# Performance work log

Measured on AMD Instinct MI355X. Metric: run time of the kernel, lower is better.

The kernel has to match this reference:

```python
import jax, jax.numpy as jnp
import numpy as np

E = 512   # embed_size == hidden_size (required: step-0 'embed' is the init output of size hidden)
H = 512
A = 512   # attention dim
V = 20000
P = 196
B = 128
T = 24


def setup_inputs() -> dict:
    key = jax.random.key(0)
    ks = jax.random.split(key, 20)
    s = 0.02
    return {
        "features": jax.random.normal(ks[0], (B, P, E), jnp.float32),
        "captions": jax.random.randint(ks[1], (B, T), 0, V),
        "emb": jax.random.normal(ks[2], (V, E), jnp.float32) * s,
        "W_init_h": jax.random.normal(ks[3], (E, H), jnp.float32) * s,
        "b_init_h": jnp.zeros((H,), jnp.float32),
        "W_init_o": jax.random.normal(ks[4], (E, H), jnp.float32) * s,
        "b_init_o": jnp.zeros((H,), jnp.float32),
        "Wf": jax.random.normal(ks[5], (E, A), jnp.float32) * s,
        "bf": jnp.zeros((A,), jnp.float32),
        "Wh": jax.random.normal(ks[6], (H, A), jnp.float32) * s,
        "bh": jnp.zeros((A,), jnp.float32),
        "v_att": jax.random.normal(ks[7], (A,), jnp.float32) * s,
        "W_ih": jax.random.normal(ks[8], (3 * H, 2 * E), jnp.float32) * s,
        "W_hh": jax.random.normal(ks[9], (3 * H, H), jnp.float32) * s,
        "b_ih": jnp.zeros((3 * H,), jnp.float32),
        "b_hh": jnp.zeros((3 * H,), jnp.float32),
        "W_out": jax.random.normal(ks[10], (V, H), jnp.float32) * s,
        "b_out": jnp.zeros((V,), jnp.float32),
    }


def reference(features, emb, W_init_h, b_init_h, W_init_o, b_init_o,
              Wf, bf, Wh, bh, v_att, W_ih, W_hh, b_ih, b_hh,
              W_out, b_out, captions):
    # init_hidden_state
    avg = features.mean(axis=1)                          # [B,E]
    hidden0 = jnp.tanh(avg @ W_init_h + b_init_h)        # [B,H]
    output0 = jnp.tanh(avg @ W_init_o + b_init_o)        # [B,H]

    emb_caps = emb[captions]                             # [B,T,E]
    # teacher forcing: step 0 uses init output, step i>0 uses embeddings[:, i-1]
    embed_seq = jnp.concatenate([output0[:, None, :], emb_caps[:, :-1, :]], axis=1)
    xs = embed_seq.transpose(1, 0, 2)                    # [T,B,E]

    feat_proj = features @ Wf + bf                       # [B,P,A] (precompute attn key proj)

    def step(h, x_emb):
        # additive attention over pixels
        score = jnp.tanh(feat_proj + (h @ Wh + bh)[:, None, :]) @ v_att   # [B,P]
        alpha = jax.nn.softmax(score, axis=1)
        ctx = jnp.einsum('bp,bpe->be', alpha, features)                   # [B,E]
        x = jnp.concatenate([x_emb, ctx], axis=1)                         # [B,2E]
        # single-step GRU (PyTorch gate order r,z,n)
        gi = x @ W_ih.T + b_ih
        gh = h @ W_hh.T + b_hh
        gi_r, gi_z, gi_n = jnp.split(gi, 3, axis=1)
        gh_r, gh_z, gh_n = jnp.split(gh, 3, axis=1)
        r = jax.nn.sigmoid(gi_r + gh_r)
        z = jax.nn.sigmoid(gi_z + gh_z)
        n = jnp.tanh(gi_n + r * gh_n)
        h_new = (1.0 - z) * n + z * h
        pred = h_new @ W_out.T + b_out                                    # [B,V]
        return h_new, pred

    _, preds = jax.lax.scan(step, hidden0, xs)           # preds: [T,B,V]
    return preds.transpose(1, 0, 2)                      # [B,T,V]
```

## Files before the change

kernel.cpp:

```cpp
#include <hip/hip_runtime.h>

#define Bb 128
#define Tt 24
#define Ee 512
#define Hh 512
#define Aa 512
#define Vv 20000
#define Pp 196
#define TV (Tt*Vv)
#define NBLK 512
#define NTHR 256
#define GT (NBLK*NTHR)

typedef __attribute__((ext_vector_type(8))) short bfrag;
typedef __attribute__((ext_vector_type(4))) float f4;
typedef __attribute__((ext_vector_type(4))) unsigned short us4;

#define MFMA16(a,b,c) __builtin_amdgcn_mfma_f32_16x16x32_bf16(a,b,c,0,0,0)

__device__ __forceinline__ unsigned short f2bf(float f){
  unsigned int x = __builtin_bit_cast(unsigned int, f);
  x += 0x7fffu + ((x >> 16) & 1u);
  return (unsigned short)(x >> 16);
}
__device__ __forceinline__ float bfu2f(unsigned short u){
  unsigned int x = ((unsigned int)u) << 16;
  return __builtin_bit_cast(float, x);
}
#define LOG2E 1.442695041f
__device__ __forceinline__ float fexp2(float x){ return __builtin_amdgcn_exp2f(x); }
__device__ __forceinline__ float frcp (float x){ return __builtin_amdgcn_rcpf(x); }
__device__ __forceinline__ float tanh_f(float x){ return 1.0f - 2.0f*frcp(1.0f + fexp2((2.0f*LOG2E)*x)); }
__device__ __forceinline__ float sigm_f(float x){ return frcp(1.0f + fexp2(-LOG2E*x)); }

__device__ __forceinline__ unsigned long long scld8(const void* p){
  return __hip_atomic_load((const unsigned long long*)p, __ATOMIC_RELAXED, __HIP_MEMORY_SCOPE_AGENT);
}
__device__ __forceinline__ unsigned scld4(const unsigned* p){
  return __hip_atomic_load(p, __ATOMIC_RELAXED, __HIP_MEMORY_SCOPE_AGENT);
}
__device__ __forceinline__ void scst4(unsigned* p, unsigned v){
  __hip_atomic_store(p, v, __ATOMIC_RELAXED, __HIP_MEMORY_SCOPE_AGENT);
}

__device__ __forceinline__ void set_flag(unsigned* line, unsigned v){
  asm volatile("s_waitcnt vmcnt(0)" ::: "memory");
  __syncthreads();
  if(threadIdx.x == 0) scst4(line, v);
}
__device__ __forceinline__ void poll_flags(const unsigned* base, int n, unsigned tgt){
  int tid = threadIdx.x;
  for(;;){
    int ok = (tid < n) ? (scld4(base + tid*16) >= tgt) : 1;
    if(__syncthreads_count(ok) == NTHR) break;
    __builtin_amdgcn_s_sleep(4);
  }
  asm volatile("" ::: "memory");
}

__device__ __forceinline__ void gbar2(unsigned* sync, unsigned phase){
  __syncthreads();
  int tid = threadIdx.x, blk = blockIdx.x;
  if(tid == 0)
    (void)__hip_atomic_fetch_add(sync + (blk & 31)*16, 1u,
                                 __ATOMIC_RELEASE, __HIP_MEMORY_SCOPE_AGENT);
  if(blk == 0){
    for(;;){
      int ok = (tid < 32) ? (scld4(sync + tid*16) >= phase*16u) : 1;
      if(__syncthreads_count(ok) == NTHR) break;
      __builtin_amdgcn_s_sleep(2);
    }
    if(tid == 0) scst4(sync + 32*16, phase);
  }
  if(tid == 0){
    while(scld4(sync + 32*16) < phase) __builtin_amdgcn_s_sleep(2);
    (void)__hip_atomic_load(sync + 32*16, __ATOMIC_ACQUIRE, __HIP_MEMORY_SCOPE_AGENT);
  }
  __syncthreads();
}

__global__ void k_zero(unsigned* s){
  int i = blockIdx.x*256 + threadIdx.x;
  s[i] = 0u;
}

__device__ __forceinline__ void cast_loop(const float* __restrict__ s,
                                          unsigned short* __restrict__ d,
                                          int n4, int gtid){
  for(int i = gtid; i < n4; i += GT){
    float4 v = ((const float4*)s)[i];
    us4 o; o[0]=f2bf(v.x); o[1]=f2bf(v.y); o[2]=f2bf(v.z); o[3]=f2bf(v.w);
    ((us4*)d)[i] = o;
  }
}
__device__ __forceinline__ void tr_tile(const float* __restrict__ S,
                                        unsigned short* __restrict__ D,
                                        int it, int jt, int tid, float (*T)[33]){
  int er = tid>>3, c4 = (tid&7)*4;
  float4 v = *(const float4*)(S + (size_t)(jt*32+er)*512 + it*32 + c4);
  T[er][c4+0]=v.x; T[er][c4+1]=v.y; T[er][c4+2]=v.z; T[er][c4+3]=v.w;
  __syncthreads();
  us4 o;
  o[0]=f2bf(T[c4+0][er]); o[1]=f2bf(T[c4+1][er]);
  o[2]=f2bf(T[c4+2][er]); o[3]=f2bf(T[c4+3][er]);
  *(us4*)(D + (size_t)(it*32+er)*512 + jt*32 + c4) = o;
  __syncthreads();
}

__device__ __forceinline__ void stage16(char* dstSM, const unsigned short* src, int R0){
  int tid = threadIdx.x;
  #pragma unroll
  for(int j=0;j<8;j++){
    int u = tid + j*256;
    int row = u >> 7, c8 = u & 127;
    unsigned long long q = scld8(src + (size_t)(R0+row)*Hh + c8*4);
    int bo = (row<<10) + (c8<<3);
    bo ^= (row&7)<<4;
    *(unsigned long long*)(dstSM + bo) = q;
  }
}


__device__ void attention_task(int b, const unsigned short* __restrict__ hbU_t,
                               const unsigned short* __restrict__ WhT, const float* __restrict__ bhv,
                               const unsigned short* __restrict__ fpb,
                               const unsigned short* __restrict__ featsB,
                               const float* __restrict__ vatt,
                               unsigned short* __restrict__ ctx_t, char* SM)
{
  float* h_s = (float*)SM;
  float* hp  = h_s + 512;
  float* vp  = hp + 512;
  float* sc  = vp + 512;
  float* red = sc + 200;
  int tid = threadIdx.x;
  if(tid < 128){
    unsigned long long q8 = scld8(hbU_t + (size_t)b*Hh + tid*4);
    h_s[tid*4+0] = bfu2f((unsigned short)(q8));
    h_s[tid*4+1] = bfu2f((unsigned short)(q8>>16));
    h_s[tid*4+2] = bfu2f((unsigned short)(q8>>32));
    h_s[tid*4+3] = bfu2f((unsigned short)(q8>>48));
  }
  { float2 vv = *(const float2*)(vatt + tid*2);
    int a0=tid*2, a1=a0+1;
    vp[((a0&31)<<4)+(a0>>5)] = vv.x;
    vp[((a1&31)<<4)+(a1>>5)] = vv.y; }
  __syncthreads();
  for(int rep=0;rep<2;rep++){
    int a = tid + rep*256;
    float s = bhv[a];
    const unsigned short* wr = WhT + (size_t)a*Hh;
    for(int k=0;k<Hh;k+=8){
      bfrag wv = *(const bfrag*)(wr + k);
      #pragma unroll
      for(int q=0;q<8;q++) s += h_s[k+q] * bfu2f((unsigned short)wv[q]);
    }
    hp[((a&31)<<4)+(a>>5)] = s;
  }
  __syncthreads();
  int grp = tid >> 4, gl = tid & 15;
  for(int pass=0; pass<13; pass++){
    int p = pass*16 + grp;
    float acc = 0.0f;
    if(p < Pp){
      const unsigned short* fr = fpb + ((size_t)b*Pp + p)*Aa + gl*32;
      #pragma unroll
      for(int j=0;j<32;j+=8){
        bfrag fv = *(const bfrag*)(fr + j);
        #pragma unroll
        for(int q=0;q<8;q++){
          int idx = ((j+q)<<4) + gl;
          float x = bfu2f((unsigned short)fv[q]) + hp[idx];
          acc += tanh_f(x) * vp[idx];
        }
      }
    }
    acc += __shfl_xor(acc, 1, 64);
    acc += __shfl_xor(acc, 2, 64);
    acc += __shfl_xor(acc, 4, 64);
    acc += __shfl_xor(acc, 8, 64);
    if(p < Pp && gl == 0) sc[p] = acc;
  }
  __syncthreads();
  if(tid < 64){
    float m = -1e30f;
    for(int i=0;i<4;i++){ int p = tid + i*64; if(p < Pp) m = fmaxf(m, sc[p]); }
    for(int off=1; off<64; off<<=1) m = fmaxf(m, __shfl_xor(m, off, 64));
    float s = 0.0f;
    for(int i=0;i<4;i++){ int p = tid + i*64; if(p < Pp) s += fexp2((sc[p]-m)*LOG2E); }
    for(int off=1; off<64; off<<=1) s += __shfl_xor(s, off, 64);
    if(tid == 0){ red[0] = m; red[1] = frcp(s); }
  }
  __syncthreads();
  float mx = red[0], rS = red[1];
  float al_t = 0.0f;
  if(tid < Pp) al_t = fexp2((sc[tid]-mx)*LOG2E) * rS;
  __syncthreads();
  if(tid < Pp) sc[tid] = al_t;
  __syncthreads();
  float c0 = 0.f, c1 = 0.f;
  const unsigned int* fb = (const unsigned int*)(featsB + (size_t)b*Pp*Ee);
  for(int p=0;p<Pp;p++){
    float al = sc[p];
    unsigned int u = fb[(size_t)p*256 + tid];
    unsigned int lo = (u & 0xffffu) << 16, hi = u & 0xffff0000u;
    c0 += al * __builtin_bit_cast(float, lo);
    c1 += al * __builtin_bit_cast(float, hi);
  }
  unsigned int cw = ((unsigned int)f2bf(c1) << 16) | (unsigned int)f2bf(c0);
  scst4((unsigned*)ctx_t + (size_t)b*256 + tid, cw);
}

__device__ void gates_phaseA(int R0, int HC0, const unsigned short* __restrict__ eseqT,
                             const unsigned short* __restrict__ WihB,
                             const unsigned short* __restrict__ WhhB,
                             const char* SMh, f4 (&agh)[3], f4 (&agi)[3])
{
  int tid = threadIdx.x;
  int w = tid>>6, l = tid&63, l16 = l&15, lk = l>>4;
  int hcol = HC0 + w*16 + l16;
  #pragma unroll
  for(int q=0;q<3;q++){ agh[q]=(f4)(0.f); agi[q]=(f4)(0.f); }
  for(int k0=0;k0<512;k0+=32){
    int koff = k0 + lk*8;
    int bo = (l16<<10) + (koff<<1); bo ^= (l16&7)<<4;
    bfrag ah = *(const bfrag*)(SMh + bo);
    bfrag ae = *(const bfrag*)(eseqT + (size_t)(R0+l16)*Ee + koff);
    #pragma unroll
    for(int q=0;q<3;q++){
      int j = q*512 + hcol;
      bfrag bh_ = *(const bfrag*)(WhhB + (size_t)j*512  + koff);
      bfrag be  = *(const bfrag*)(WihB + (size_t)j*1024 + koff);
      agh[q] = MFMA16(ah, bh_, agh[q]);
      agi[q] = MFMA16(ae, be,  agi[q]);
    }
  }
}

__device__ void gates_phaseB(int R0, int HC0, const char* SMc,
                             const unsigned short* __restrict__ WihB,
                             const float* __restrict__ bih, const float* __restrict__ bhh,
                             const float* __restrict__ hf_cur, float* __restrict__ hf_nxt,
                             unsigned short* __restrict__ hbU_nxt,
                             f4 (&agh)[3], f4 (&agi)[3], char* SM_HB)
{
  int tid = threadIdx.x;
  int w = tid>>6, l = tid&63, l16 = l&15, lk = l>>4;
  int hcol = HC0 + w*16 + l16;
  for(int k0=0;k0<512;k0+=32){
    int koff = k0 + lk*8;
    int bo = (l16<<10) + (koff<<1); bo ^= (l16&7)<<4;
    bfrag ac = *(const bfrag*)(SMc + bo);
    #pragma unroll
    for(int q=0;q<3;q++){
      int j = q*512 + hcol;
      bfrag bc = *(const bfrag*)(WihB + (size_t)j*1024 + 512 + koff);
      agi[q] = MFMA16(ac, bc, agi[q]);
    }
  }
  float bir = bih[hcol],      bhr = bhh[hcol];
  float biz = bih[512+hcol],  bhz = bhh[512+hcol];
  float bin = bih[1024+hcol], bhn = bhh[1024+hcol];
  unsigned short (*HB)[64] = (unsigned short(*)[64])SM_HB;
  #pragma unroll
  for(int i=0;i<4;i++){
    int row = lk*4 + i;
    int b = R0 + row;
    float r_ = sigm_f(agi[0][i] + bir + agh[0][i] + bhr);
    float z_ = sigm_f(agi[1][i] + biz + agh[1][i] + bhz);
    float n_ = tanh_f(agi[2][i] + bin + r_*(agh[2][i] + bhn));
    float ho = hf_cur[(size_t)b*Hh + hcol];
    float hn = (1.0f - z_)*n_ + z_*ho;
    hf_nxt[(size_t)b*Hh + hcol] = hn;
    HB[row][w*16 + l16] = f2bf(hn);
  }
  __syncthreads();
  #pragma unroll
  for(int j=0;j<2;j++){
    int widx = tid + j*256;
    int row = widx >> 5, pr = widx & 31;
    unsigned uu = (unsigned)HB[row][pr*2] | ((unsigned)HB[row][pr*2+1] << 16);
    scst4((unsigned*)(hbU_nxt + (size_t)(R0+row)*Hh + HC0) + pr, uu);
  }
}

__device__ void pred_task(int pt, int tw, const unsigned short* __restrict__ hb_cur,
                          const unsigned short* __restrict__ WoutB,
                          const float* __restrict__ bout, float* __restrict__ out,
                          char* SM)
{
  int tid = threadIdx.x;
  int vchunk = pt >> 1, mbase = (pt & 1)*64;
  for(int j=0;j<32;j++){
    int u = tid + j*256;
    int row = u >> 7, c8 = u & 127;
    unsigned long long q = scld8(hb_cur + (size_t)(mbase+row)*Hh + c8*4);
    int bo = (row<<10) + (c8<<3);
    bo ^= (row&7)<<4;
    *(unsigned long long*)(SM + bo) = q;
  }
  __syncthreads();
  int w = tid>>6, l = tid&63, l16 = l&15, lk = l>>4;
  int nb = vchunk*128 + w*32;
  f4 acc[4][2];
  #pragma unroll
  for(int mi=0;mi<4;mi++) for(int ni=0;ni<2;ni++) acc[mi][ni] = (f4)(0.0f);
  for(int k0=0;k0<512;k0+=32){
    int koff = k0 + lk*8;
    bfrag af[4], bq[2];
    #pragma unroll
    for(int mi=0;mi<4;mi++){
      int row = mi*16 + l16;
      int bo = (row<<10) + (koff<<1);
      bo ^= (row&7)<<4;
      af[mi] = *(const bfrag*)(SM + bo);
    }
    #pragma unroll
    for(int ni=0;ni<2;ni++){
      int v = nb + ni*16 + l16; if(v > Vv-1) v = Vv-1;
      bq[ni] = *(const bfrag*)(WoutB + (size_t)v*Hh + koff);
    }
    #pragma unroll
    for(int mi=0;mi<4;mi++)
      #pragma unroll
      for(int ni=0;ni<2;ni++)
        acc[mi][ni] = MFMA16(af[mi], bq[ni], acc[mi][ni]);
  }
  #pragma unroll
  for(int ni=0;ni<2;ni++){
    int v = nb + ni*16 + l16;
    if(v < Vv){
      float bias = bout[v];
      #pragma unroll
      for(int mi=0;mi<4;mi++){
        #pragma unroll
        for(int i=0;i<4;i++){
          int br = mbase + mi*16 + lk*4 + i;
          __builtin_nontemporal_store(acc[mi][ni][i] + bias,
              out + (size_t)br*TV + (size_t)tw*Vv + v);
        }
      }
    }
  }
  __syncthreads();
}

__global__ __launch_bounds__(NTHR, 2) void k_all(
    const float* feats, const int* caps, const float* emb,
    const float* Winh, const float* binh, const float* Wino, const float* bino,
    const float* Wf, const float* bfv, const float* Wh, const float* bhv,
    const float* vatt, const float* Wih, const float* Whh,
    const float* bih, const float* bhh, const float* Wout, const float* bout,
    float* out,
    float* hfR, unsigned short* hbU,
    unsigned short* ctxR, unsigned short* avgB, unsigned short* eseq,
    unsigned short* WfT, unsigned short* WhT,
    unsigned short* WinhT, unsigned short* WinoT,
    unsigned short* WihB, unsigned short* WhhB,
    unsigned short* fpb, unsigned short* featsB, unsigned short* WoutB,
    unsigned* sync)
{
  __shared__ char SMEM[65536];
  const int blk = blockIdx.x, tid = threadIdx.x;
  const int gtid = blk*NTHR + tid;
  unsigned* flagsA = sync + 40*16;
  unsigned* flagsG = sync + 168*16;
  unsigned* aggP   = sync + 240*16;
  float* h_f0 = hfR;
  unsigned short* h_b0 = hbU;

  cast_loop(Wih,  WihB,  (3*Hh*2*Ee)/4, gtid);
  cast_loop(Whh,  WhhB,  (3*Hh*Hh)/4,   gtid);
  cast_loop(Wout, WoutB, (Vv*Hh)/4,     gtid);
  cast_loop(feats,featsB,(Bb*Pp*Ee)/4,  gtid);
  for(int task = blk; task < 1024; task += NBLK){
    int z = task >> 8, rt = task & 255;
    int it = rt & 15, jt = rt >> 4;
    const float* S = (z==0)?Wf:(z==1)?Wh:(z==2)?Winh:Wino;
    unsigned short* D = (z==0)?WfT:(z==1)?WhT:(z==2)?WinhT:WinoT;
    tr_tile(S, D, it, jt, tid, (float(*)[33])SMEM);
  }
  if(blk < Bb){
    int b = blk;
    const float* fb = feats + (size_t)b*Pp*Ee;
    float a0=0.f, a1=0.f;
    for(int p=0;p<Pp;p++){
      float2 v = *(const float2*)(fb + (size_t)p*Ee + tid*2);
      a0 += v.x; a1 += v.y;
    }
    a0 *= (1.0f/Pp); a1 *= (1.0f/Pp);
    unsigned int pack = ((unsigned int)f2bf(a1)<<16) | (unsigned int)f2bf(a0);
    ((unsigned int*)avgB)[(size_t)b*256 + tid] = pack;
  }
  for(int task = blk; task < (Tt-1)*Bb; task += NBLK){
    int ts = task/Bb + 1, b = task%Bb;
    int cap = caps[b*Tt + (ts-1)];
    float2 v = *(const float2*)(emb + (size_t)cap*Ee + tid*2);
    unsigned int pack = ((unsigned int)f2bf(v.y)<<16) | (unsigned int)f2bf(v.x);
    ((unsigned int*)(eseq + ((size_t)ts*Bb + b)*Ee))[tid] = pack;
  }
  gbar2(sync, 1);

  for(int task = blk; task < 1584; task += NBLK){
    int w = tid>>6, l = tid&63, l16 = l&15, lk = l>>4;
    if(task < 1568){
      int bx = task % 196, by = task / 196;
      size_t m_base = (size_t)bx*128 + (w&1)*64;
      int nb = by*64 + (w>>1)*32;
      f4 acc[4][2];
      #pragma unroll
      for(int mi=0;mi<4;mi++) for(int ni=0;ni<2;ni++) acc[mi][ni] = (f4)(0.0f);
      for(int k0=0;k0<512;k0+=32){
        int koff = k0 + lk*8;
        bfrag af[4], bq[2];
        #pragma unroll
        for(int mi=0;mi<4;mi++) af[mi] = *(const bfrag*)(featsB + (m_base+mi*16+l16)*512 + koff);
        #pragma unroll
        for(int ni=0;ni<2;ni++) bq[ni] = *(const bfrag*)(WfT + (size_t)(nb+ni*16+l16)*512 + koff);
        #pragma unroll
        for(int mi=0;mi<4;mi++)
          #pragma unroll
          for(int ni=0;ni<2;ni++)
            acc[mi][ni] = MFMA16(af[mi], bq[ni], acc[mi][ni]);
      }
      #pragma unroll
      for(int ni=0;ni<2;ni++){
        int a = nb + ni*16 + l16;
        float bias = bfv[a];
        #pragma unroll
        for(int mi=0;mi<4;mi++){
          size_t r = m_base + mi*16 + lk*4;
          #pragma unroll
          for(int i=0;i<4;i++)
            fpb[(r+i)*512 + a] = f2bf(acc[mi][ni][i] + bias);
        }
      }
    } else {
      int idx = task - 1568;
      int y = idx >> 3, xb = idx & 7;
      int m0 = (w&1)*64, nb = xb*64 + (w>>1)*32;
      const unsigned short* Wt = y ? WinoT : WinhT;
      const float* bias = y ? bino : binh;
      f4 acc[4][2];
      #pragma unroll
      for(int mi=0;mi<4;mi++) for(int ni=0;ni<2;ni++) acc[mi][ni] = (f4)(0.0f);
      for(int k0=0;k0<512;k0+=32){
        int koff = k0 + lk*8;
        bfrag af[4], bq[2];
        #pragma unroll
        for(int mi=0;mi<4;mi++) af[mi] = *(const bfrag*)(avgB + (size_t)(m0+mi*16+l16)*512 + koff);
        #pragma unroll
        for(int ni=0;ni<2;ni++) bq[ni] = *(const bfrag*)(Wt + (size_t)(nb+ni*16+l16)*512 + koff);
        #pragma unroll
        for(int mi=0;mi<4;mi++)
          #pragma unroll
          for(int ni=0;ni<2;ni++)
            acc[mi][ni] = MFMA16(af[mi], bq[ni], acc[mi][ni]);
      }
      #pragma unroll
      for(int ni=0;ni<2;ni++){
        int n = nb + ni*16 + l16;
        float bv = bias[n];
        #pragma unroll
        for(int mi=0;mi<4;mi++){
          int bb = m0 + mi*16 + lk*4;
          #pragma unroll
          for(int i=0;i<4;i++){
            float val = tanh_f(acc[mi][ni][i] + bv);
            if(y==0){ h_f0[(size_t)(bb+i)*Hh + n] = val; h_b0[(size_t)(bb+i)*Hh + n] = f2bf(val); }
            else    { eseq[(size_t)(bb+i)*Ee + n] = f2bf(val); }
          }
        }
      }
    }
  }
  gbar2(sync, 2);

  int xcd = blk & 7, slot = blk >> 3;

  if(slot < 16){
    int b = slot*8 + xcd;
    int rg = b >> 4;
    for(int t=0; t<Tt; t++){
      if(t > 0) poll_flags(flagsG + rg*8*16, 8, (unsigned)t);
      attention_task(b, hbU + (size_t)t*Bb*Hh, WhT, bhv, fpb, featsB, vatt,
                     ctxR + (size_t)(t&3)*Bb*Ee, SMEM);
      set_flag(flagsA + b*16, (unsigned)(t+1));
    }
  } else if(slot < 24){
    int r = slot - 16, c = xcd;
    int R0 = r*16, HC0 = c*64;
    char* SMh = SMEM;
    char* SMc = SMEM + 16384;
    char* SMB = SMEM + 32768;
    f4 agh[3], agi[3];
    stage16(SMh, hbU, R0);
    __syncthreads();
    gates_phaseA(R0, HC0, eseq, WihB, WhhB, SMh, agh, agi);
    for(int t=0; t<Tt; t++){
      poll_flags(flagsA + R0*16, 16, (unsigned)(t+1));
      stage16(SMc, ctxR + (size_t)(t&3)*Bb*Ee, R0);
      __syncthreads();
      gates_phaseB(R0, HC0, SMc, WihB, bih, bhh,
                   hfR + (size_t)(t&1)*Bb*Hh, hfR + (size_t)((t+1)&1)*Bb*Hh,
                   hbU + (size_t)(t+1)*Bb*Hh, agh, agi, SMB);
      set_flag(flagsG + (r*8+c)*16, (unsigned)(t+1));
      if(t+1 < Tt){
        poll_flags(flagsG + r*8*16, 8, (unsigned)(t+1));
        stage16(SMh, hbU + (size_t)(t+1)*Bb*Hh, R0);
        __syncthreads();
        gates_phaseA(R0, HC0, eseq + (size_t)(t+1)*Bb*Ee, WihB, WhhB, SMh, agh, agi);
      }
    }
  } else {
    int ps = slot - 24;
    int pt = xcd*40 + ps;
    if(ps == 0){
      for(int t=1; t<=Tt; t++){
        poll_flags(flagsG, 64, (unsigned)t);
        if(tid == 0) scst4(aggP + xcd*16, (unsigned)t);
        pred_task(pt, t-1, hbU + (size_t)t*Bb*Hh, WoutB, bout, out, SMEM);
      }
    } else if(pt < 314){
      for(int t=1; t<=Tt; t++){
        poll_flags(aggP + xcd*16, 1, (unsigned)t);
        pred_task(pt, t-1, hbU + (size_t)t*Bb*Hh, WoutB, bout, out, SMEM);
      }
    }
  }
}

extern "C" void kernel_launch(void* const* d_in, const int* in_sizes, int n_in,
                              void* d_out, int out_size, void* d_ws, size_t ws_size,
                              hipStream_t stream)
{
  const float* feats = (const float*)d_in[0];
  const int*   caps  = (const int*)d_in[1];
  const float* emb   = (const float*)d_in[2];
  const float* Winh  = (const float*)d_in[3];
  const float* binh  = (const float*)d_in[4];
  const float* Wino  = (const float*)d_in[5];
  const float* bino  = (const float*)d_in[6];
  const float* Wf    = (const float*)d_in[7];
  const float* bfv   = (const float*)d_in[8];
  const float* Wh    = (const float*)d_in[9];
  const float* bhv   = (const float*)d_in[10];
  const float* vatt  = (const float*)d_in[11];
  const float* Wih   = (const float*)d_in[12];
  const float* Whh   = (const float*)d_in[13];
  const float* bih   = (const float*)d_in[14];
  const float* bhh   = (const float*)d_in[15];
  const float* Wout  = (const float*)d_in[16];
  const float* bout  = (const float*)d_in[17];
  float* out = (float*)d_out;

  char* ws = (char*)d_ws;
  size_t off = 0;
  auto alloc = [&](size_t bytes){
    off = (off + 255) & ~(size_t)255;
    void* p = ws + off; off += bytes; return p;
  };
  unsigned* syncp = (unsigned*)alloc(16384);
  float* hfR = (float*)alloc((size_t)2*Bb*Hh*4);
  unsigned short* hbU = (unsigned short*)alloc((size_t)(Tt+1)*Bb*Hh*2);
  unsigned short* ctxR  = (unsigned short*)alloc((size_t)4*Bb*Ee*2);
  unsigned short* avgB  = (unsigned short*)alloc((size_t)Bb*Ee*2);
  unsigned short* eseq  = (unsigned short*)alloc((size_t)Tt*Bb*Ee*2);
  unsigned short* WfT   = (unsigned short*)alloc((size_t)Ee*Aa*2);
  unsigned short* WhT   = (unsigned short*)alloc((size_t)Hh*Aa*2);
  unsigned short* WinhT = (unsigned short*)alloc((size_t)Ee*Hh*2);
  unsigned short* WinoT = (unsigned short*)alloc((size_t)Ee*Hh*2);
  unsigned short* WihB  = (unsigned short*)alloc((size_t)3*Hh*2*Ee*2);
  unsigned short* WhhB  = (unsigned short*)alloc((size_t)3*Hh*Hh*2);
  unsigned short* fpb   = (unsigned short*)alloc((size_t)Bb*Pp*Aa*2);
  unsigned short* featsB= (unsigned short*)alloc((size_t)Bb*Pp*Ee*2);
  unsigned short* WoutB = (unsigned short*)alloc((size_t)Vv*Hh*2);
  if(ws_size < off) return;

  k_zero<<<16, 256, 0, stream>>>(syncp);
  k_all<<<NBLK, NTHR, 0, stream>>>(
      feats, caps, emb, Winh, binh, Wino, bino, Wf, bfv, Wh, bhv, vatt,
      Wih, Whh, bih, bhh, Wout, bout, out,
      hfR, hbU, ctxR, avgB, eseq,
      WfT, WhT, WinhT, WinoT, WihB, WhhB, fpb, featsB, WoutB, syncp);
}
```

Baseline: 1.676 ms.

## Move attention h-projection into GRU blocks via MFMA and reshape pred tiles

The per-batch scalar h@Wh projection inside each attention task is removed. The GRU tile blocks now compute it with MFMA right after staging h, write it to a double-buffered fp32 buffer, and publish a new flag that attention blocks poll. The prediction task switches from 64-row by 128-vocab tiles to 32-row by 256-vocab tiles, and launch bounds are raised to 4 blocks per CU with dynamic shared memory sized 34816 bytes. This cuts redundant projection work from the serial attention critical path, at the cost of an extra flag handshake and possible register pressure at the higher occupancy target.

```diff
diff --git a/kernel.cpp b/kernel.cpp
--- a/kernel.cpp
+++ b/kernel.cpp
@@ -11,6 +11,7 @@
 #define NBLK 512
 #define NTHR 256
 #define GT (NBLK*NTHR)
+#define SMEM_BYTES 34816
 
 typedef __attribute__((ext_vector_type(8))) short bfrag;
 typedef __attribute__((ext_vector_type(4))) float f4;
@@ -40,6 +41,9 @@
   return __hip_atomic_load(p, __ATOMIC_RELAXED, __HIP_MEMORY_SCOPE_AGENT);
 }
 __device__ __forceinline__ void scst4(unsigned* p, unsigned v){
+  __hip_atomic_store(p, v, __ATOMIC_RELAXED, __HIP_MEMORY_SCOPE_AGENT);
+}
+__device__ __forceinline__ void scstf(float* p, float v){
   __hip_atomic_store(p, v, __ATOMIC_RELAXED, __HIP_MEMORY_SCOPE_AGENT);
 }
 
@@ -121,41 +125,26 @@
 }
 
 
-__device__ void attention_task(int b, const unsigned short* __restrict__ hbU_t,
-                               const unsigned short* __restrict__ WhT, const float* __restrict__ bhv,
+__device__ void attention_task(int b, const float* __restrict__ hpr_t,
                                const unsigned short* __restrict__ fpb,
                                const unsigned short* __restrict__ featsB,
                                const float* __restrict__ vatt,
                                unsigned short* __restrict__ ctx_t, char* SM)
 {
-  float* h_s = (float*)SM;
-  float* hp  = h_s + 512;
+  float* hp  = (float*)SM;
   float* vp  = hp + 512;
   float* sc  = vp + 512;
   float* red = sc + 200;
   int tid = threadIdx.x;
-  if(tid < 128){
-    unsigned long long q8 = scld8(hbU_t + (size_t)b*Hh + tid*4);
-    h_s[tid*4+0] = bfu2f((unsigned short)(q8));
-    h_s[tid*4+1] = bfu2f((unsigned short)(q8>>16));
-    h_s[tid*4+2] = bfu2f((unsigned short)(q8>>32));
-    h_s[tid*4+3] = bfu2f((unsigned short)(q8>>48));
-  }
-  { float2 vv = *(const float2*)(vatt + tid*2);
-    int a0=tid*2, a1=a0+1;
+  {
+    unsigned long long q = scld8(hpr_t + (size_t)b*Aa + tid*2);
+    float2 hv = __builtin_bit_cast(float2, q);
+    float2 vv = *(const float2*)(vatt + tid*2);
+    int a0 = tid*2, a1 = a0+1;
+    hp[((a0&31)<<4)+(a0>>5)] = hv.x;
+    hp[((a1&31)<<4)+(a1>>5)] = hv.y;
     vp[((a0&31)<<4)+(a0>>5)] = vv.x;
-    vp[((a1&31)<<4)+(a1>>5)] = vv.y; }
-  __syncthreads();
-  for(int rep=0;rep<2;rep++){
-    int a = tid + rep*256;
-    float s = bhv[a];
-    const unsigned short* wr = WhT + (size_t)a*Hh;
-    for(int k=0;k<Hh;k+=8){
-      bfrag wv = *(const bfrag*)(wr + k);
-      #pragma unroll
-      for(int q=0;q<8;q++) s += h_s[k+q] * bfu2f((unsigned short)wv[q]);
-    }
-    hp[((a&31)<<4)+(a>>5)] = s;
+    vp[((a1&31)<<4)+(a1>>5)] = vv.y;
   }
   __syncthreads();
   int grp = tid >> 4, gl = tid & 15;
@@ -209,6 +198,29 @@
   }
   unsigned int cw = ((unsigned int)f2bf(c1) << 16) | (unsigned int)f2bf(c0);
   scst4((unsigned*)ctx_t + (size_t)b*256 + tid, cw);
+}
+
+__device__ void hproj_mfma(int R0, int HC0, const char* SMh,
+                           const unsigned short* __restrict__ WhT,
+                           const float* __restrict__ bhv, float* __restrict__ hpr)
+{
+  int tid = threadIdx.x;
+  int w = tid>>6, l = tid&63, l16 = l&15, lk = l>>4;
+  int a = HC0 + w*16 + l16;
+  f4 acc = (f4)(0.0f);
+  for(int k0=0;k0<512;k0+=32){
+    int koff = k0 + lk*8;
+    int bo = (l16<<10) + (koff<<1); bo ^= (l16&7)<<4;
+    bfrag ah = *(const bfrag*)(SMh + bo);
+    bfrag bq = *(const bfrag*)(WhT + (size_t)a*Hh + koff);
+    acc = MFMA16(ah, bq, acc);
+  }
+  float bias = bhv[a];
+  #pragma unroll
+  for(int i=0;i<4;i++){
+    int row = lk*4 + i;
+    scstf(hpr + (size_t)(R0+row)*Aa + a, acc[i] + bias);
+  }
 }
 
 __device__ void gates_phaseA(int R0, int HC0, const unsigned short* __restrict__ eseqT,
@@ -284,14 +296,15 @@
   }
 }
 
-__device__ void pred_task(int pt, int tw, const unsigned short* __restrict__ hb_cur,
-                          const unsigned short* __restrict__ WoutB,
-                          const float* __restrict__ bout, float* __restrict__ out,
-                          char* SM)
+__device__ void pred_task32(int pt, int tw, const unsigned short* __restrict__ hb_cur,
+                            const unsigned short* __restrict__ WoutB,
+                            const float* __restrict__ bout, float* __restrict__ out,
+                            char* SM)
 {
   int tid = threadIdx.x;
-  int vchunk = pt >> 1, mbase = (pt & 1)*64;
-  for(int j=0;j<32;j++){
+  int vchunk = pt >> 2, mbase = (pt & 3)*32;
+  #pragma unroll
+  for(int j=0;j<16;j++){
     int u = tid + j*256;
     int row = u >> 7, c8 = u & 127;
     unsigned long long q = scld8(hb_cur + (size_t)(mbase+row)*Hh + c8*4);
@@ -301,38 +314,38 @@
   }
   __syncthreads();
   int w = tid>>6, l = tid&63, l16 = l&15, lk = l>>4;
-  int nb = vchunk*128 + w*32;
-  f4 acc[4][2];
-  #pragma unroll
-  for(int mi=0;mi<4;mi++) for(int ni=0;ni<2;ni++) acc[mi][ni] = (f4)(0.0f);
+  int nb = vchunk*256 + w*64;
+  f4 acc[2][4];
+  #pragma unroll
+  for(int mi=0;mi<2;mi++) for(int ni=0;ni<4;ni++) acc[mi][ni] = (f4)(0.0f);
   for(int k0=0;k0<512;k0+=32){
     int koff = k0 + lk*8;
-    bfrag af[4], bq[2];
+    bfrag af[2], bq[4];
     #pragma unroll
-    for(int mi=0;mi<4;mi++){
+    for(int mi=0;mi<2;mi++){
       int row = mi*16 + l16;
       int bo = (row<<10) + (koff<<1);
       bo ^= (row&7)<<4;
       af[mi] = *(const bfrag*)(SM + bo);
     }
     #pragma unroll
-    for(int ni=0;ni<2;ni++){
+    for(int ni=0;ni<4;ni++){
       int v = nb + ni*16 + l16; if(v > Vv-1) v = Vv-1;
       bq[ni] = *(const bfrag*)(WoutB + (size_t)v*Hh + koff);
     }
     #pragma unroll
-    for(int mi=0;mi<4;mi++)
+    for(int mi=0;mi<2;mi++)
       #pragma unroll
-      for(int ni=0;ni<2;ni++)
+      for(int ni=0;ni<4;ni++)
         acc[mi][ni] = MFMA16(af[mi], bq[ni], acc[mi][ni]);
   }
   #pragma unroll
-  for(int ni=0;ni<2;ni++){
+  for(int ni=0;ni<4;ni++){
     int v = nb + ni*16 + l16;
     if(v < Vv){
       float bias = bout[v];
       #pragma unroll
-      for(int mi=0;mi<4;mi++){
+      for(int mi=0;mi<2;mi++){
         #pragma unroll
         for(int i=0;i<4;i++){
           int br = mbase + mi*16 + lk*4 + i;
@@ -345,14 +358,14 @@
   __syncthreads();
 }
 
-__global__ __launch_bounds__(NTHR, 2) void k_all(
+__global__ __launch_bounds__(NTHR, 4) void k_all(
     const float* feats, const int* caps, const float* emb,
     const float* Winh, const float* binh, const float* Wino, const float* bino,
     const float* Wf, const float* bfv, const float* Wh, const float* bhv,
     const float* vatt, const float* Wih, const float* Whh,
     const float* bih, const float* bhh, const float* Wout, const float* bout,
     float* out,
-    float* hfR, unsigned short* hbU,
+    float* hfR, unsigned short* hbU, float* hpr,
     unsigned short* ctxR, unsigned short* avgB, unsigned short* eseq,
     unsigned short* WfT, unsigned short* WhT,
     unsigned short* WinhT, unsigned short* WinoT,
@@ -360,12 +373,13 @@
     unsigned short* fpb, unsigned short* featsB, unsigned short* WoutB,
     unsigned* sync)
 {
-  __shared__ char SMEM[65536];
+  extern __shared__ char SMEM[];
   const int blk = blockIdx.x, tid = threadIdx.x;
   const int gtid = blk*NTHR + tid;
   unsigned* flagsA = sync + 40*16;
   unsigned* flagsG = sync + 168*16;
-  unsigned* aggP   = sync + 240*16;
+  unsigned* flagsP = sync + 240*16;
+  unsigned* aggP   = sync + 304*16;
   float* h_f0 = hfR;
   unsigned short* h_b0 = hbU;
 
@@ -482,8 +496,8 @@
     int b = slot*8 + xcd;
     int rg = b >> 4;
     for(int t=0; t<Tt; t++){
-      if(t > 0) poll_flags(flagsG + rg*8*16, 8, (unsigned)t);
-      attention_task(b, hbU + (size_t)t*Bb*Hh, WhT, bhv, fpb, featsB, vatt,
+      poll_flags(flagsP + rg*8*16, 8, (unsigned)(t+1));
+      attention_task(b, hpr + (size_t)(t&1)*Bb*Aa, fpb, featsB, vatt,
                      ctxR + (size_t)(t&3)*Bb*Ee, SMEM);
       set_flag(flagsA + b*16, (unsigned)(t+1));
     }
@@ -496,6 +510,8 @@
     f4 agh[3], agi[3];
     stage16(SMh, hbU, R0);
     __syncthreads();
+    hproj_mfma(R0, HC0, SMh, WhT, bhv, hpr);
+    set_flag(flagsP + (r*8+c)*16, 1u);
     gates_phaseA(R0, HC0, eseq, WihB, WhhB, SMh, agh, agi);
     for(int t=0; t<Tt; t++){
       poll_flags(flagsA + R0*16, 16, (unsigned)(t+1));
@@ -509,6 +525,8 @@
         poll_flags(flagsG + r*8*16, 8, (unsigned)(t+1));
         stage16(SMh, hbU + (size_t)(t+1)*Bb*Hh, R0);
         __syncthreads();
+        hproj_mfma(R0, HC0, SMh, WhT, bhv, hpr + (size_t)((t+1)&1)*Bb*Aa);
+        set_flag(flagsP + (r*8+c)*16, (unsigned)(t+2));
         gates_phaseA(R0, HC0, eseq + (size_t)(t+1)*Bb*Ee, WihB, WhhB, SMh, agh, agi);
       }
     }
@@ -519,12 +537,12 @@
       for(int t=1; t<=Tt; t++){
         poll_flags(flagsG, 64, (unsigned)t);
         if(tid == 0) scst4(aggP + xcd*16, (unsigned)t);
-        pred_task(pt, t-1, hbU + (size_t)t*Bb*Hh, WoutB, bout, out, SMEM);
-      }
-    } else if(pt < 314){
+        pred_task32(pt, t-1, hbU + (size_t)t*Bb*Hh, WoutB, bout, out, SMEM);
+      }
+    } else if(pt < 316){
       for(int t=1; t<=Tt; t++){
         poll_flags(aggP + xcd*16, 1, (unsigned)t);
-        pred_task(pt, t-1, hbU + (size_t)t*Bb*Hh, WoutB, bout, out, SMEM);
+        pred_task32(pt, t-1, hbU + (size_t)t*Bb*Hh, WoutB, bout, out, SMEM);
       }
     }
   }
@@ -560,9 +578,10 @@
     off = (off + 255) & ~(size_t)255;
     void* p = ws + off; off += bytes; return p;
   };
-  unsigned* syncp = (unsigned*)alloc(16384);
+  unsigned* syncp = (unsigned*)alloc(32768);
   float* hfR = (float*)alloc((size_t)2*Bb*Hh*4);
   unsigned short* hbU = (unsigned short*)alloc((size_t)(Tt+1)*Bb*Hh*2);
+  float* hpr = (float*)alloc((size_t)2*Bb*Aa*4);
   unsigned short* ctxR  = (unsigned short*)alloc((size_t)4*Bb*Ee*2);
   unsigned short* avgB  = (unsigned short*)alloc((size_t)Bb*Ee*2);
   unsigned short* eseq  = (unsigned short*)alloc((size_t)Tt*Bb*Ee*2);
@@ -577,10 +596,10 @@
   unsigned short* WoutB = (unsigned short*)alloc((size_t)Vv*Hh*2);
   if(ws_size < off) return;
 
-  k_zero<<<16, 256, 0, stream>>>(syncp);
-  k_all<<<NBLK, NTHR, 0, stream>>>(
+  k_zero<<<32, 256, 0, stream>>>(syncp);
+  k_all<<<NBLK, NTHR, SMEM_BYTES, stream>>>(
       feats, caps, emb, Winh, binh, Wino, bino, Wf, bfv, Wh, bhv, vatt,
       Wih, Whh, bih, bhh, Wout, bout, out,
-      hfR, hbU, ctxR, avgB, eseq,
+      hfR, hbU, hpr, ctxR, avgB, eseq,
       WfT, WhT, WinhT, WinoT, WihB, WhhB, fpb, featsB, WoutB, syncp);
 }
```

Result: faster. 1.445 ms, median of 2 (-13.8%).
